# Performance work log

Measured on AMD Instinct MI355X. Metric: run time of the kernel, lower is better.

Reference implementation:

```python
import jax, jax.numpy as jnp
from jax import lax
import numpy as np

NEG_SLOPE = 0.01  # PyTorch LeakyReLU default


def setup_inputs() -> dict:
    key = jax.random.key(0)
    ks = jax.random.split(key, 7)
    B, Ns, T, C = 32, 512, 128, 25
    proj_dim, H = 20, 25
    s_lin = 1.0 / np.sqrt(C)
    s_gru = 1.0 / np.sqrt(H)
    return {
        "x": jax.random.normal(ks[0], (B, Ns, T, C), jnp.float32),
        "W1": jax.random.uniform(ks[1], (proj_dim, C), jnp.float32, -s_lin, s_lin),
        "b1": jax.random.uniform(ks[2], (proj_dim,), jnp.float32, -s_lin, s_lin),
        "W_ih": jax.random.uniform(ks[3], (3 * H, proj_dim), jnp.float32, -s_gru, s_gru),
        "W_hh": jax.random.uniform(ks[4], (3 * H, H), jnp.float32, -s_gru, s_gru),
        "b_ih": jax.random.uniform(ks[5], (3 * H,), jnp.float32, -s_gru, s_gru),
        "b_hh": jax.random.uniform(ks[6], (3 * H,), jnp.float32, -s_gru, s_gru),
    }


def reference(x, W1, b1, W_ih, W_hh, b_ih, b_hh):
    # Linear + LeakyReLU projection: [B, Ns, T, 25] -> [B, Ns, T, proj_dim]
    p = jnp.einsum("bntc,pc->bntp", x, W1) + b1
    p = jnp.where(p >= 0, p, NEG_SLOPE * p)

    B, Ns, T, P = p.shape
    H = W_hh.shape[1]
    p = p.reshape(B * Ns, T, P)

    # Precompute input-side gate pre-activations for all timesteps: [N, T, 3H]
    gx = jnp.einsum("ntp,gp->ntg", p, W_ih) + b_ih
    gx = jnp.swapaxes(gx, 0, 1)  # [T, N, 3H] for scan

    def step(h, gx_t):
        gh = h @ W_hh.T + b_hh  # [N, 3H]
        xr, xz, xn = jnp.split(gx_t, 3, axis=-1)
        hr, hz, hn = jnp.split(gh, 3, axis=-1)
        r = jax.nn.sigmoid(xr + hr)
        z = jax.nn.sigmoid(xz + hz)
        n = jnp.tanh(xn + r * hn)
        h_new = (1.0 - z) * n + z * h
        return h_new, None

    h0 = jnp.zeros((B * Ns, H), p.dtype)
    hT, _ = lax.scan(step, h0, gx)
    return hT.reshape(B, Ns, H)
```

## Files before the change

kernel.cpp:

```cpp
#include <hip/hip_runtime.h>


typedef __bf16 bf16x8 __attribute__((ext_vector_type(8)));
typedef float  f32x4  __attribute__((ext_vector_type(4)));

#define TT 128
#define CC 25
#define PP 20
#define HH 25
#define NSEQ 16384
#define S  36
#define MFMA __builtin_amdgcn_mfma_f32_16x16x32_bf16

__device__ __forceinline__ void split2(float f, __bf16& hi, __bf16& lo) {
    hi = (__bf16)f;
    lo = (__bf16)(f - (float)hi);
}
__device__ __forceinline__ float sigm(float v) { return 1.f / (1.f + __expf(-v)); }

__global__ __launch_bounds__(64, 1) void gru_mfma_t(
    const float* __restrict__ x,   const float* __restrict__ W1,
    const float* __restrict__ b1,  const float* __restrict__ Wih,
    const float* __restrict__ Whh, const float* __restrict__ bih,
    const float* __restrict__ bhh, float* __restrict__ out)
{
    __shared__ float sp[16 * S];
    __shared__ float sh[2][16 * S];

    const int lane = threadIdx.x;
    const int m = lane & 15, q = lane >> 4;
    const int n0 = blockIdx.x * 16;

    for (int idx = lane; idx < 16 * S; idx += 64) {
        sp[idx] = 0.f; sh[0][idx] = 0.f; sh[1][idx] = 0.f;
    }
    __syncthreads();
    if (lane < 16) {
        sp[lane * S + PP]    = 1.0f;
        sh[0][lane * S + HH] = 1.0f;
        sh[1][lane * S + HH] = 1.0f;
    }
    __syncthreads();

    bf16x8 WihH[6], WihL[6], WhhH[6], WhhL[6], W1H[2], W1L[2];
    #pragma unroll
    for (int tt = 0; tt < 6; ++tt) {
        const int g = tt >> 1;
        const int u = (tt & 1) * 16 + m;
        const bool uv = (u < HH);
        const int row = g * HH + u;
        bf16x8 ih, il, hh, hl;
        #pragma unroll
        for (int j = 0; j < 8; ++j) {
            const int k = q * 8 + j;
            float vih = 0.f, vhh = 0.f;
            if (uv) {
                if (k < PP)       vih = Wih[row * PP + k];
                else if (k == PP) vih = bih[row];
                if (k < HH)       vhh = Whh[row * HH + k];
                else if (k == HH) vhh = bhh[row];
            }
            __bf16 a, b;
            split2(vih, a, b); ih[j] = a; il[j] = b;
            split2(vhh, a, b); hh[j] = a; hl[j] = b;
        }
        WihH[tt] = ih; WihL[tt] = il; WhhH[tt] = hh; WhhL[tt] = hl;
    }
    #pragma unroll
    for (int tt = 0; tt < 2; ++tt) {
        const int u = tt * 16 + m;
        const bool uv = (u < PP);
        bf16x8 h8, l8;
        #pragma unroll
        for (int j = 0; j < 8; ++j) {
            const int k = q * 8 + j;
            float v = 0.f;
            if (uv) {
                if (k < CC)       v = W1[u * CC + k];
                else if (k == CC) v = b1[u];
            }
            __bf16 a, b; split2(v, a, b); h8[j] = a; l8[j] = b;
        }
        W1H[tt] = h8; W1L[tt] = l8;
    }

    const float* xrow = x + (size_t)(n0 + m) * (TT * CC);
    float xc[8];
    #pragma unroll
    for (int j = 0; j < 8; ++j) {
        const int k = q * 8 + j;
        xc[j] = (k < CC) ? xrow[k] : (k == CC ? 1.0f : 0.f);
    }

    struct GX { f32x4 r[2], z[2], n[2]; };

    auto compute_gx = [&](int tn, GX& g) {
        bf16x8 xH, xL;
        #pragma unroll
        for (int j = 0; j < 8; ++j) { __bf16 a,b; split2(xc[j],a,b); xH[j]=a; xL[j]=b; }

        {
            const float* xr = xrow + tn * CC;
            #pragma unroll
            for (int j = 0; j < 8; ++j) {
                const int k = q * 8 + j;
                if (k < CC) xc[j] = xr[k];
            }
        }

        f32x4 p0 = {0.f,0.f,0.f,0.f}, p1 = {0.f,0.f,0.f,0.f};
        p0 = MFMA(W1H[0], xH, p0, 0,0,0);
        p0 = MFMA(W1H[0], xL, p0, 0,0,0);
        p0 = MFMA(W1L[0], xH, p0, 0,0,0);
        p1 = MFMA(W1H[1], xH, p1, 0,0,0);
        p1 = MFMA(W1H[1], xL, p1, 0,0,0);
        p1 = MFMA(W1L[1], xH, p1, 0,0,0);
        #pragma unroll
        for (int r = 0; r < 4; ++r) {
            p0[r] = (p0[r] >= 0.f) ? p0[r] : 0.01f * p0[r];
            p1[r] = (p1[r] >= 0.f) ? p1[r] : 0.01f * p1[r];
        }

        *(f32x4*)(sp + m * S + 4 * q) = p0;
        if (q == 0) *(f32x4*)(sp + m * S + 16) = p1;

        f32x4 pa = ((const f32x4*)(sp + m * S + 8 * q))[0];
        f32x4 pb = ((const f32x4*)(sp + m * S + 8 * q))[1];
        bf16x8 pH, pL;
        #pragma unroll
        for (int j = 0; j < 4; ++j) {
            __bf16 a, b;
            split2(pa[j], a, b); pH[j]   = a; pL[j]   = b;
            split2(pb[j], a, b); pH[4+j] = a; pL[4+j] = b;
        }

        #pragma unroll
        for (int tp = 0; tp < 2; ++tp) {
            f32x4 acc = {0.f,0.f,0.f,0.f};
            acc = MFMA(WihH[tp], pH, acc, 0,0,0);
            acc = MFMA(WihH[tp], pL, acc, 0,0,0);
            acc = MFMA(WihL[tp], pH, acc, 0,0,0);
            g.r[tp] = acc;
            f32x4 az = {0.f,0.f,0.f,0.f};
            az = MFMA(WihH[2+tp], pH, az, 0,0,0);
            az = MFMA(WihH[2+tp], pL, az, 0,0,0);
            az = MFMA(WihL[2+tp], pH, az, 0,0,0);
            g.z[tp] = az;
            f32x4 an = {0.f,0.f,0.f,0.f};
            an = MFMA(WihH[4+tp], pH, an, 0,0,0);
            an = MFMA(WihH[4+tp], pL, an, 0,0,0);
            an = MFMA(WihL[4+tp], pH, an, 0,0,0);
            g.n[tp] = an;
        }
    };

    float ho[2][4] = {{0.f,0.f,0.f,0.f},{0.f,0.f,0.f,0.f}};

    auto gru_step = [&](int t, const GX& g) {
        const float* hrow = sh[t & 1] + m * S + 8 * q;
        f32x4 ha = ((const f32x4*)hrow)[0];
        f32x4 hb = ((const f32x4*)hrow)[1];
        bf16x8 hH, hL;
        #pragma unroll
        for (int j = 0; j < 4; ++j) {
            __bf16 a, b;
            split2(ha[j], a, b); hH[j]   = a; hL[j]   = b;
            split2(hb[j], a, b); hH[4+j] = a; hL[4+j] = b;
        }
        f32x4 aR[2], aZ[2], aHn[2];
        #pragma unroll
        for (int tp = 0; tp < 2; ++tp) {
            f32x4 acc = g.r[tp];
            acc = MFMA(WhhH[tp], hH, acc, 0,0,0);
            acc = MFMA(WhhH[tp], hL, acc, 0,0,0);
            acc = MFMA(WhhL[tp], hH, acc, 0,0,0);
            aR[tp] = acc;
            f32x4 az = g.z[tp];
            az = MFMA(WhhH[2+tp], hH, az, 0,0,0);
            az = MFMA(WhhH[2+tp], hL, az, 0,0,0);
            az = MFMA(WhhL[2+tp], hH, az, 0,0,0);
            aZ[tp] = az;
            f32x4 ah = {0.f,0.f,0.f,0.f};
            ah = MFMA(WhhH[4+tp], hH, ah, 0,0,0);
            ah = MFMA(WhhH[4+tp], hL, ah, 0,0,0);
            ah = MFMA(WhhL[4+tp], hH, ah, 0,0,0);
            aHn[tp] = ah;
        }
        #pragma unroll
        for (int tp = 0; tp < 2; ++tp) {
            f32x4 hv;
            #pragma unroll
            for (int r = 0; r < 4; ++r) {
                const float rg = sigm(aR[tp][r]);
                const float zg = sigm(aZ[tp][r]);
                const float nv = g.n[tp][r] + rg * aHn[tp][r];
                const float e  = __expf(-2.f * nv);
                const float ng = 2.f / (1.f + e) - 1.f;
                const float h2 = zg * (ho[tp][r] - ng) + ng;
                ho[tp][r] = h2; hv[r] = h2;
            }
            float* dst = sh[(t + 1) & 1] + m * S + tp * 16 + 4 * q;
            if (tp == 0) {
                *(f32x4*)dst = hv;
            } else {
                if (q < 2)       *(f32x4*)dst = hv;
                else if (q == 2) dst[0] = hv[0];
            }
        }
    };

    GX A, B;
    compute_gx(1, A);

    for (int t = 0; t < TT; t += 2) {
        const int t2 = (t + 2 < TT) ? t + 2 : TT - 1;
        const int t3 = (t + 3 < TT) ? t + 3 : TT - 1;
        compute_gx(t2, B);
        gru_step(t, A);
        compute_gx(t3, A);
        gru_step(t + 1, B);
    }

    float* orow = out + (size_t)(n0 + m) * HH;
    #pragma unroll
    for (int tp = 0; tp < 2; ++tp) {
        #pragma unroll
        for (int r = 0; r < 4; ++r) {
            const int u = tp * 16 + 4 * q + r;
            if (u < HH) orow[u] = ho[tp][r];
        }
    }
}

extern "C" void kernel_launch(void* const* d_in, const int* in_sizes, int n_in,
                              void* d_out, int out_size, void* d_ws, size_t ws_size,
                              hipStream_t stream) {
    const float* x   = (const float*)d_in[0];
    const float* W1  = (const float*)d_in[1];
    const float* b1  = (const float*)d_in[2];
    const float* Wih = (const float*)d_in[3];
    const float* Whh = (const float*)d_in[4];
    const float* bih = (const float*)d_in[5];
    const float* bhh = (const float*)d_in[6];
    float* out = (float*)d_out;

    gru_mfma_t<<<NSEQ / 16, 64, 0, stream>>>(x, W1, b1, Wih, Whh, bih, bhh, out);
}
```

Measured before the change: 421.7 us.

## Split GRU into producer/consumer warps exchanging gate inputs via shared memory

Result: no change. 421.7 us (+0.0%).

```diff
diff --git a/kernel.cpp b/kernel.cpp
--- a/kernel.cpp
+++ b/kernel.cpp
@@ -18,7 +18,7 @@
 }
 __device__ __forceinline__ float sigm(float v) { return 1.f / (1.f + __expf(-v)); }
 
-__global__ __launch_bounds__(64, 1) void gru_mfma_t(
+__global__ __launch_bounds__(128, 2) void gru_pc(
     const float* __restrict__ x,   const float* __restrict__ W1,
     const float* __restrict__ b1,  const float* __restrict__ Wih,
     const float* __restrict__ Whh, const float* __restrict__ bih,
@@ -26,80 +26,81 @@
 {
     __shared__ float sp[16 * S];
     __shared__ float sh[2][16 * S];
-
-    const int lane = threadIdx.x;
+    __shared__ f32x4 sgx[2][3][2][4][16];
+
+    const int tid  = threadIdx.x;
+    const int wid  = tid >> 6;
+    const bool pw  = (wid == 0);
+    const int lane = tid & 63;
     const int m = lane & 15, q = lane >> 4;
     const int n0 = blockIdx.x * 16;
 
-    for (int idx = lane; idx < 16 * S; idx += 64) {
+    for (int idx = tid; idx < 16 * S; idx += 128) {
         sp[idx] = 0.f; sh[0][idx] = 0.f; sh[1][idx] = 0.f;
     }
     __syncthreads();
-    if (lane < 16) {
-        sp[lane * S + PP]    = 1.0f;
-        sh[0][lane * S + HH] = 1.0f;
-        sh[1][lane * S + HH] = 1.0f;
+    if (tid < 16) {
+        sp[tid * S + PP]    = 1.0f;
+        sh[0][tid * S + HH] = 1.0f;
+        sh[1][tid * S + HH] = 1.0f;
     }
     __syncthreads();
 
-    bf16x8 WihH[6], WihL[6], WhhH[6], WhhL[6], W1H[2], W1L[2];
-    #pragma unroll
-    for (int tt = 0; tt < 6; ++tt) {
-        const int g = tt >> 1;
-        const int u = (tt & 1) * 16 + m;
-        const bool uv = (u < HH);
-        const int row = g * HH + u;
-        bf16x8 ih, il, hh, hl;
-        #pragma unroll
-        for (int j = 0; j < 8; ++j) {
-            const int k = q * 8 + j;
-            float vih = 0.f, vhh = 0.f;
-            if (uv) {
-                if (k < PP)       vih = Wih[row * PP + k];
-                else if (k == PP) vih = bih[row];
-                if (k < HH)       vhh = Whh[row * HH + k];
-                else if (k == HH) vhh = bhh[row];
-            }
-            __bf16 a, b;
-            split2(vih, a, b); ih[j] = a; il[j] = b;
-            split2(vhh, a, b); hh[j] = a; hl[j] = b;
-        }
-        WihH[tt] = ih; WihL[tt] = il; WhhH[tt] = hh; WhhL[tt] = hl;
-    }
-    #pragma unroll
-    for (int tt = 0; tt < 2; ++tt) {
-        const int u = tt * 16 + m;
-        const bool uv = (u < PP);
-        bf16x8 h8, l8;
-        #pragma unroll
-        for (int j = 0; j < 8; ++j) {
-            const int k = q * 8 + j;
-            float v = 0.f;
-            if (uv) {
-                if (k < CC)       v = W1[u * CC + k];
-                else if (k == CC) v = b1[u];
-            }
-            __bf16 a, b; split2(v, a, b); h8[j] = a; l8[j] = b;
-        }
-        W1H[tt] = h8; W1L[tt] = l8;
+    bf16x8 WgH[6], WgL[6], WpH[2], WpL[2];
+    {
+        const float* Ws = pw ? Wih : Whh;
+        const float* bs = pw ? bih : bhh;
+        const int kd    = pw ? PP  : HH;
+        #pragma unroll
+        for (int tt = 0; tt < 6; ++tt) {
+            const int g = tt >> 1;
+            const int u = (tt & 1) * 16 + m;
+            const bool uv = (u < HH);
+            const int row = g * HH + u;
+            bf16x8 h8, l8;
+            #pragma unroll
+            for (int j = 0; j < 8; ++j) {
+                const int k = q * 8 + j;
+                float v = 0.f;
+                if (uv) {
+                    if (k < kd)       v = Ws[row * kd + k];
+                    else if (k == kd) v = bs[row];
+                }
+                __bf16 a, b; split2(v, a, b); h8[j] = a; l8[j] = b;
+            }
+            WgH[tt] = h8; WgL[tt] = l8;
+        }
+    }
+    if (pw) {
+        #pragma unroll
+        for (int tt = 0; tt < 2; ++tt) {
+            const int u = tt * 16 + m;
+            const bool uv = (u < PP);
+            bf16x8 h8, l8;
+            #pragma unroll
+            for (int j = 0; j < 8; ++j) {
+                const int k = q * 8 + j;
+                float v = 0.f;
+                if (uv) {
+                    if (k < CC)       v = W1[u * CC + k];
+                    else if (k == CC) v = b1[u];
+                }
+                __bf16 a, b; split2(v, a, b); h8[j] = a; l8[j] = b;
+            }
+            WpH[tt] = h8; WpL[tt] = l8;
+        }
     }
 
     const float* xrow = x + (size_t)(n0 + m) * (TT * CC);
     float xc[8];
-    #pragma unroll
-    for (int j = 0; j < 8; ++j) {
-        const int k = q * 8 + j;
-        xc[j] = (k < CC) ? xrow[k] : (k == CC ? 1.0f : 0.f);
-    }
-
-    struct GX { f32x4 r[2], z[2], n[2]; };
-
-    auto compute_gx = [&](int tn, GX& g) {
+
+    auto produce = [&](int tc) {
         bf16x8 xH, xL;
         #pragma unroll
         for (int j = 0; j < 8; ++j) { __bf16 a,b; split2(xc[j],a,b); xH[j]=a; xL[j]=b; }
 
         {
+            const int tn = (tc + 1 < TT) ? tc + 1 : TT - 1;
             const float* xr = xrow + tn * CC;
             #pragma unroll
             for (int j = 0; j < 8; ++j) {
@@ -109,12 +110,12 @@
         }
 
         f32x4 p0 = {0.f,0.f,0.f,0.f}, p1 = {0.f,0.f,0.f,0.f};
-        p0 = MFMA(W1H[0], xH, p0, 0,0,0);
-        p0 = MFMA(W1H[0], xL, p0, 0,0,0);
-        p0 = MFMA(W1L[0], xH, p0, 0,0,0);
-        p1 = MFMA(W1H[1], xH, p1, 0,0,0);
-        p1 = MFMA(W1H[1], xL, p1, 0,0,0);
-        p1 = MFMA(W1L[1], xH, p1, 0,0,0);
+        p0 = MFMA(WpH[0], xH, p0, 0,0,0);
+        p0 = MFMA(WpH[0], xL, p0, 0,0,0);
+        p0 = MFMA(WpL[0], xH, p0, 0,0,0);
+        p1 = MFMA(WpH[1], xH, p1, 0,0,0);
+        p1 = MFMA(WpH[1], xL, p1, 0,0,0);
+        p1 = MFMA(WpL[1], xH, p1, 0,0,0);
         #pragma unroll
         for (int r = 0; r < 4; ++r) {
             p0[r] = (p0[r] >= 0.f) ? p0[r] : 0.01f * p0[r];
@@ -134,29 +135,30 @@
             split2(pb[j], a, b); pH[4+j] = a; pL[4+j] = b;
         }
 
+        const int s = tc & 1;
         #pragma unroll
         for (int tp = 0; tp < 2; ++tp) {
             f32x4 acc = {0.f,0.f,0.f,0.f};
-            acc = MFMA(WihH[tp], pH, acc, 0,0,0);
-            acc = MFMA(WihH[tp], pL, acc, 0,0,0);
-            acc = MFMA(WihL[tp], pH, acc, 0,0,0);
-            g.r[tp] = acc;
+            acc = MFMA(WgH[tp], pH, acc, 0,0,0);
+            acc = MFMA(WgH[tp], pL, acc, 0,0,0);
+            acc = MFMA(WgL[tp], pH, acc, 0,0,0);
+            sgx[s][0][tp][q][m] = acc;
             f32x4 az = {0.f,0.f,0.f,0.f};
-            az = MFMA(WihH[2+tp], pH, az, 0,0,0);
-            az = MFMA(WihH[2+tp], pL, az, 0,0,0);
-            az = MFMA(WihL[2+tp], pH, az, 0,0,0);
-            g.z[tp] = az;
+            az = MFMA(WgH[2+tp], pH, az, 0,0,0);
+            az = MFMA(WgH[2+tp], pL, az, 0,0,0);
+            az = MFMA(WgL[2+tp], pH, az, 0,0,0);
+            sgx[s][1][tp][q][m] = az;
             f32x4 an = {0.f,0.f,0.f,0.f};
-            an = MFMA(WihH[4+tp], pH, an, 0,0,0);
-            an = MFMA(WihH[4+tp], pL, an, 0,0,0);
-            an = MFMA(WihL[4+tp], pH, an, 0,0,0);
-            g.n[tp] = an;
+            an = MFMA(WgH[4+tp], pH, an, 0,0,0);
+            an = MFMA(WgH[4+tp], pL, an, 0,0,0);
+            an = MFMA(WgL[4+tp], pH, an, 0,0,0);
+            sgx[s][2][tp][q][m] = an;
         }
     };
 
     float ho[2][4] = {{0.f,0.f,0.f,0.f},{0.f,0.f,0.f,0.f}};
 
-    auto gru_step = [&](int t, const GX& g) {
+    auto consume = [&](int t) {
         const float* hrow = sh[t & 1] + m * S + 8 * q;
         f32x4 ha = ((const f32x4*)hrow)[0];
         f32x4 hb = ((const f32x4*)hrow)[1];
@@ -167,23 +169,25 @@
             split2(ha[j], a, b); hH[j]   = a; hL[j]   = b;
             split2(hb[j], a, b); hH[4+j] = a; hL[4+j] = b;
         }
-        f32x4 aR[2], aZ[2], aHn[2];
-        #pragma unroll
-        for (int tp = 0; tp < 2; ++tp) {
-            f32x4 acc = g.r[tp];
-            acc = MFMA(WhhH[tp], hH, acc, 0,0,0);
-            acc = MFMA(WhhH[tp], hL, acc, 0,0,0);
-            acc = MFMA(WhhL[tp], hH, acc, 0,0,0);
+        const int s = t & 1;
+        f32x4 aR[2], aZ[2], aHn[2], gN[2];
+        #pragma unroll
+        for (int tp = 0; tp < 2; ++tp) {
+            f32x4 acc = sgx[s][0][tp][q][m];
+            acc = MFMA(WgH[tp], hH, acc, 0,0,0);
+            acc = MFMA(WgH[tp], hL, acc, 0,0,0);
+            acc = MFMA(WgL[tp], hH, acc, 0,0,0);
             aR[tp] = acc;
-            f32x4 az = g.z[tp];
-            az = MFMA(WhhH[2+tp], hH, az, 0,0,0);
-            az = MFMA(WhhH[2+tp], hL, az, 0,0,0);
-            az = MFMA(WhhL[2+tp], hH, az, 0,0,0);
+            f32x4 az = sgx[s][1][tp][q][m];
+            az = MFMA(WgH[2+tp], hH, az, 0,0,0);
+            az = MFMA(WgH[2+tp], hL, az, 0,0,0);
+            az = MFMA(WgL[2+tp], hH, az, 0,0,0);
             aZ[tp] = az;
+            gN[tp] = sgx[s][2][tp][q][m];
             f32x4 ah = {0.f,0.f,0.f,0.f};
-            ah = MFMA(WhhH[4+tp], hH, ah, 0,0,0);
-            ah = MFMA(WhhH[4+tp], hL, ah, 0,0,0);
-            ah = MFMA(WhhL[4+tp], hH, ah, 0,0,0);
+            ah = MFMA(WgH[4+tp], hH, ah, 0,0,0);
+            ah = MFMA(WgH[4+tp], hL, ah, 0,0,0);
+            ah = MFMA(WgL[4+tp], hH, ah, 0,0,0);
             aHn[tp] = ah;
         }
         #pragma unroll
@@ -193,7 +197,7 @@
             for (int r = 0; r < 4; ++r) {
                 const float rg = sigm(aR[tp][r]);
                 const float zg = sigm(aZ[tp][r]);
-                const float nv = g.n[tp][r] + rg * aHn[tp][r];
+                const float nv = gN[tp][r] + rg * aHn[tp][r];
                 const float e  = __expf(-2.f * nv);
                 const float ng = 2.f / (1.f + e) - 1.f;
                 const float h2 = zg * (ho[tp][r] - ng) + ng;
@@ -209,25 +213,34 @@
         }
     };
 
-    GX A, B;
-    compute_gx(1, A);
-
-    for (int t = 0; t < TT; t += 2) {
-        const int t2 = (t + 2 < TT) ? t + 2 : TT - 1;
-        const int t3 = (t + 3 < TT) ? t + 3 : TT - 1;
-        compute_gx(t2, B);
-        gru_step(t, A);
-        compute_gx(t3, A);
-        gru_step(t + 1, B);
-    }
-
-    float* orow = out + (size_t)(n0 + m) * HH;
-    #pragma unroll
-    for (int tp = 0; tp < 2; ++tp) {
-        #pragma unroll
-        for (int r = 0; r < 4; ++r) {
-            const int u = tp * 16 + 4 * q + r;
-            if (u < HH) orow[u] = ho[tp][r];
+    if (pw) {
+        #pragma unroll
+        for (int j = 0; j < 8; ++j) {
+            const int k = q * 8 + j;
+            xc[j] = (k < CC) ? xrow[k] : (k == CC ? 1.0f : 0.f);
+        }
+        produce(0);
+    }
+    __syncthreads();
+
+    for (int t = 0; t < TT; ++t) {
+        if (pw) {
+            if (t + 1 < TT) produce(t + 1);
+        } else {
+            consume(t);
+        }
+        __syncthreads();
+    }
+
+    if (!pw) {
+        float* orow = out + (size_t)(n0 + m) * HH;
+        #pragma unroll
+        for (int tp = 0; tp < 2; ++tp) {
+            #pragma unroll
+            for (int r = 0; r < 4; ++r) {
+                const int u = tp * 16 + 4 * q + r;
+                if (u < HH) orow[u] = ho[tp][r];
+            }
         }
     }
 }
@@ -244,5 +257,5 @@
     const float* bhh = (const float*)d_in[6];
     float* out = (float*)d_out;
 
-    gru_mfma_t<<<NSEQ / 16, 64, 0, stream>>>(x, W1, b1, Wih, Whh, bih, bhh, out);
+    gru_pc<<<NSEQ / 16, 128, 0, stream>>>(x, W1, b1, Wih, Whh, bih, bhh, out);
 }
```
